# Kernel tuning notes

Hardware: AMD Instinct MI355X
Metric: run time of the kernel (lower is better)

Reference implementation:

```python
import jax, jax.numpy as jnp
import numpy as np

NUM_HEADS = 16


def setup_inputs() -> dict:
    key = jax.random.key(0)
    k1, k2, k3 = jax.random.split(key, 3)
    S, B, E = 2048, 4, 1024
    std = float(np.sqrt(2.0 / (E + E)))
    query = jax.random.normal(k1, (S, B, E), dtype=jnp.float32)
    in_proj_weight = jax.random.normal(k2, (3 * E, E), dtype=jnp.float32) * std
    in_proj_bias = jnp.zeros((3 * E,), dtype=jnp.float32)
    out_proj_weight = jax.random.normal(k3, (E, E), dtype=jnp.float32) * std
    out_proj_bias = jnp.zeros((E,), dtype=jnp.float32)
    return {
        "query": query,
        "in_proj_weight": in_proj_weight,
        "in_proj_bias": in_proj_bias,
        "out_proj_weight": out_proj_weight,
        "out_proj_bias": out_proj_bias,
    }


def reference(query, in_proj_weight, in_proj_bias, out_proj_weight, out_proj_bias):
    S, B, E = query.shape
    H = NUM_HEADS
    hd = E // H
    scale = hd ** -0.5
    # fused QKV projection: [S, B, 3E]
    lin = jnp.einsum("sbe,fe->sbf", query, in_proj_weight) + in_proj_bias
    # torch layout: view(S, B*H, 3, hd) -> interleaved [h, {q,k,v}, hd]
    lin = lin.reshape(S, B * H, 3, hd)
    q = lin[:, :, 0, :]  # [S, B*H, hd]
    k = lin[:, :, 1, :]
    v = lin[:, :, 2, :]
    # scores: [B*H, S_q, S_k]
    scores = jnp.einsum("sbd,tbd->bst", q, k) * scale
    attn = jax.nn.softmax(scores.astype(jnp.float32), axis=-1).astype(scores.dtype)
    # context: [S, B*H, hd] -> [S, B, E]
    ctx = jnp.einsum("bst,tbd->sbd", attn, v).reshape(S, B, E)
    out = jnp.einsum("sbe,fe->sbf", ctx, out_proj_weight) + out_proj_bias
    return out
```

## Files before the change

### kernel.cpp

```cpp
#include <hip/hip_runtime.h>
#include <hip/hip_bf16.h>

typedef __hip_bfloat16 bf16;
typedef __attribute__((ext_vector_type(8))) short short8;
typedef __attribute__((ext_vector_type(4))) float floatx4;

#define GLD_LDS(g, l) __builtin_amdgcn_global_load_lds( \
    (const __attribute__((address_space(1))) void*)(g), \
    (__attribute__((address_space(3))) void*)(l), 16, 0, 0)

#define CS 0.18033688f

__device__ __forceinline__ float fast_exp2(float x)
{
    const float fl = floorf(x);
    const float t  = x - fl;
    float p = 1.0f + t * (0.69583f + t * (0.22606f + t * 0.078024f));
    union { float f; int i; } u;
    u.f = p;
    u.i += ((int)fl) << 23;
    return u.f;
}

__global__ __launch_bounds__(256)
void cvt3_kernel(const float* __restrict__ q,  bf16* __restrict__ qo,
                 const float* __restrict__ w1, bf16* __restrict__ w1o,
                 const float* __restrict__ w2, bf16* __restrict__ w2o)
{
    const int i = blockIdx.x * 256 + threadIdx.x;
    const float* src; bf16* dst; long off;
    if (i < 1048576)       { src = q;  dst = qo;  off = (long)i * 8; }
    else if (i < 1441792)  { src = w1; dst = w1o; off = (long)(i - 1048576) * 8; }
    else                   { src = w2; dst = w2o; off = (long)(i - 1441792) * 8; }
    floatx4 a = *(const floatx4*)(src + off);
    floatx4 b = *(const floatx4*)(src + off + 4);
    short8 h;
    #pragma unroll
    for (int e = 0; e < 4; ++e) {
        union { bf16 v; short s; } u0, u1;
        u0.v = __float2bfloat16(a[e]); h[e]     = u0.s;
        u1.v = __float2bfloat16(b[e]); h[e + 4] = u1.s;
    }
    *(short8*)(dst + off) = h;
}

__device__ __forceinline__ void stage_f32(const float* __restrict__ src, int ld,
                                          bf16* lds, int t)
{
    const int sr = t >> 1;
    const int sc = (t & 1) * 16;
    const float* g = src + (long)sr * ld + sc;
    floatx4 f[4];
    #pragma unroll
    for (int i = 0; i < 4; ++i) f[i] = *(const floatx4*)(g + i * 4);
    short8 h[2];
    #pragma unroll
    for (int v = 0; v < 2; ++v)
        #pragma unroll
        for (int e = 0; e < 8; ++e) {
            union { bf16 b; short s; } u;
            u.b = __float2bfloat16(f[v * 2 + (e >> 2)][e & 3]);
            h[v][e] = u.s;
        }
    *(short8*)(lds + sr * 32 + sc)     = h[0];
    *(short8*)(lds + sr * 32 + sc + 8) = h[1];
}

template<int EPI, int AF32, int BF32>
__global__ __launch_bounds__(256, 2)
void gemm_bt(const void* __restrict__ Ap, const void* __restrict__ Bp,
             const float* __restrict__ bias,
             void* __restrict__ o0, bf16* __restrict__ o1, bf16* __restrict__ o2,
             int K, int N)
{
    __shared__ __align__(16) bf16 lA[2][128 * 32];
    __shared__ __align__(16) bf16 lB[2][128 * 32];

    const int t    = threadIdx.x;
    const int lane = t & 63;
    const int w    = t >> 6;

    const int nb   = N >> 7;
    const int lin  = blockIdx.y * nb + blockIdx.x;
    const int cpx  = (nb << 6) >> 3;
    const int swz  = (lin & 7) * cpx + (lin >> 3);
    const int mBase = (swz / nb) * 128;
    const int nBase = (swz % nb) * 128;

    const int wr = (w >> 1) * 64;
    const int wc = (w & 1) * 64;

    const int rowL = t >> 2;
    const int colL = (t & 3) * 8;
    const bf16* gA0 = (const bf16*)Ap + (long)(mBase + rowL) * K + colL;
    const bf16* gA1 = (const bf16*)Ap + (long)(mBase + rowL + 64) * K + colL;
    const bf16* gB0 = (const bf16*)Bp + (long)(nBase + rowL) * K + colL;
    const bf16* gB1 = (const bf16*)Bp + (long)(nBase + rowL + 64) * K + colL;
    const int ldst = w * 1024;

    floatx4 acc[4][4] = {};

    auto stage = [&](int buf, int k0) __attribute__((always_inline)) {
        if constexpr (AF32) {
            stage_f32((const float*)Ap + (long)mBase * K + k0, K, lA[buf], t);
        } else {
            GLD_LDS(gA0 + k0, (char*)lA[buf] + ldst);
            GLD_LDS(gA1 + k0, (char*)lA[buf] + ldst + 4096);
        }
        if constexpr (BF32) {
            stage_f32((const float*)Bp + (long)nBase * K + k0, K, lB[buf], t);
        } else {
            GLD_LDS(gB0 + k0, (char*)lB[buf] + ldst);
            GLD_LDS(gB1 + k0, (char*)lB[buf] + ldst + 4096);
        }
    };

    auto compute = [&](int buf) __attribute__((always_inline)) {
        short8 af[4], bfr[4];
        #pragma unroll
        for (int m = 0; m < 4; ++m)
            af[m] = *(const short8*)(lA[buf] + (wr + m * 16 + (lane & 15)) * 32 + (lane >> 4) * 8);
        #pragma unroll
        for (int n = 0; n < 4; ++n)
            bfr[n] = *(const short8*)(lB[buf] + (wc + n * 16 + (lane & 15)) * 32 + (lane >> 4) * 8);
        #pragma unroll
        for (int m = 0; m < 4; ++m)
            #pragma unroll
            for (int n = 0; n < 4; ++n)
                acc[m][n] = __builtin_amdgcn_mfma_f32_16x16x32_bf16(af[m], bfr[n], acc[m][n], 0, 0, 0);
    };

    stage(0, 0);
    asm volatile("s_waitcnt vmcnt(0)" ::: "memory");
    __syncthreads();

    for (int k0 = 0; k0 < K; k0 += 64) {
        if (k0 + 32 < K) stage(1, k0 + 32);
        compute(0);
        asm volatile("s_waitcnt vmcnt(0)" ::: "memory");
        __syncthreads();
        if (k0 + 32 < K) {
            if (k0 + 64 < K) stage(0, k0 + 64);
            compute(1);
            asm volatile("s_waitcnt vmcnt(0)" ::: "memory");
            __syncthreads();
        }
    }

    #pragma unroll
    for (int m = 0; m < 4; ++m) {
        #pragma unroll
        for (int n = 0; n < 4; ++n) {
            const int col = nBase + wc + n * 16 + (lane & 15);
            const int r0  = mBase + wr + m * 16 + ((lane >> 4) << 2);
            const float bv = bias[col];
            if constexpr (EPI == 0) {
                const int h   = col / 192;
                const int rem = col % 192;
                const int qkv = rem >> 6;
                const int d   = rem & 63;
                #pragma unroll
                for (int j = 0; j < 4; ++j) {
                    const int r = r0 + j;
                    const int s = r >> 2;
                    const int b = r & 3;
                    const float v = acc[m][n][j] + bv;
                    if (qkv == 0)
                        ((bf16*)o0)[(((((b << 4) + h) << 11) + s) << 6) + d] =
                            __float2bfloat16(v * CS);
                    else if (qkv == 1)
                        o1[(((((b << 4) + h) << 11) + s) << 6) + d] = __float2bfloat16(v);
                    else
                        o2[((((b << 4) + h) << 17)) + (d << 11) + s] = __float2bfloat16(v);
                }
            } else {
                #pragma unroll
                for (int j = 0; j < 4; ++j)
                    ((float*)o0)[(long)(r0 + j) * N + col] = acc[m][n][j] + bv;
            }
        }
    }
}

__global__ __launch_bounds__(256, 2)
void attn_kernel(const bf16* __restrict__ Q, const bf16* __restrict__ Kg,
                 const bf16* __restrict__ Vt, bf16* __restrict__ Ctx)
{
    __shared__ __align__(16) bf16 lK[2][64 * 64];
    __shared__ __align__(16) bf16 lV[2][64 * 64];

    const int t    = threadIdx.x;
    const int lane = t & 63;
    const int w    = t >> 6;
    const int f    = lane & 15;
    const int g    = lane >> 4;
    const int lin  = blockIdx.x;
    const int bh   = (lin & 7) | (((lin >> 8) & 7) << 3);
    const int q0   = ((lin >> 3) & 31) * 64 + w * 16;
    const long hb  = (long)bh * 2048 * 64;
    const bf16* Qh = Q  + hb;
    const bf16* Kh = Kg + hb;
    const bf16* Vh = Vt + hb;

    const bf16* kSrc[2]; const bf16* vSrc[2];
    #pragma unroll
    for (int i = 0; i < 2; ++i) {
        const int X = t * 16 + i * 4096;
        const int r = X >> 7;
        const int c = (X & 127) ^ ((r & 7) << 4);
        const int sr = (r & 3) | ((r & 16) >> 2) | ((r & 12) << 1) | (r & 32);
        kSrc[i] = Kh + sr * 64 + (c >> 1);
        vSrc[i] = Vh + r * 2048 + (c >> 1);
    }
    const int ldst = w * 1024;

    const int rb0 = (f * 128 + g * 16)      ^ ((f & 7) << 4);
    const int rb1 = (f * 128 + g * 16 + 64) ^ ((f & 7) << 4);

    short8 qf[2];
    #pragma unroll
    for (int kk = 0; kk < 2; ++kk)
        qf[kk] = *(const short8*)(Qh + (q0 + f) * 64 + kk * 32 + g * 8);

    short8 ones;
    #pragma unroll
    for (int e = 0; e < 8; ++e) ones[e] = (short)0x3F80;

    floatx4 o[4] = {};
    floatx4 dn = {};

    #pragma unroll
    for (int i = 0; i < 2; ++i) {
        GLD_LDS(kSrc[i], (char*)lK[0] + ldst + i * 4096);
        GLD_LDS(vSrc[i], (char*)lV[0] + ldst + i * 4096);
    }
    asm volatile("s_waitcnt vmcnt(0)" ::: "memory");
    __syncthreads();

    auto tile = [&](const bf16* curK, const bf16* curV,
                    bf16* nxtK, bf16* nxtV, int t0) __attribute__((always_inline)) {
        if (t0 + 64 < 2048) {
            const int ko = (t0 + 64) * 64;
            const int vo = t0 + 64;
            #pragma unroll
            for (int i = 0; i < 2; ++i) {
                GLD_LDS(kSrc[i] + ko, (char*)nxtK + ldst + i * 4096);
                GLD_LDS(vSrc[i] + vo, (char*)nxtV + ldst + i * 4096);
            }
        }

        short8 kf[4][2];
        #pragma unroll
        for (int n = 0; n < 4; ++n) {
            kf[n][0] = *(const short8*)((const char*)curK + rb0 + n * 2048);
            kf[n][1] = *(const short8*)((const char*)curK + rb1 + n * 2048);
        }

        floatx4 sa2[4] = {};
        __builtin_amdgcn_s_setprio(1);
        #pragma unroll
        for (int n = 0; n < 4; ++n)
            #pragma unroll
            for (int kk = 0; kk < 2; ++kk)
                sa2[n] = __builtin_amdgcn_mfma_f32_16x16x32_bf16(kf[n][kk], qf[kk], sa2[n], 0, 0, 0);
        __builtin_amdgcn_s_setprio(0);

        short8 vf[4][2];
        #pragma unroll
        for (int n2 = 0; n2 < 4; ++n2) {
            vf[n2][0] = *(const short8*)((const char*)curV + rb0 + n2 * 2048);
            vf[n2][1] = *(const short8*)((const char*)curV + rb1 + n2 * 2048);
        }

        short8 pf[2];
        #pragma unroll
        for (int kk = 0; kk < 2; ++kk) {
            union { int i4[4]; short8 s8; } u;
            #pragma unroll
            for (int v = 0; v < 4; ++v) {
                const int n = 2 * kk + (v >> 1);
                const int e = 2 * (v & 1);
                float2 pr;
                pr.x = fast_exp2(sa2[n][e]);
                pr.y = fast_exp2(sa2[n][e + 1]);
                __hip_bfloat162 pb = __float22bfloat162_rn(pr);
                u.i4[v] = *reinterpret_cast<int*>(&pb);
            }
            pf[kk] = u.s8;
        }

        __builtin_amdgcn_s_setprio(1);
        #pragma unroll
        for (int n2 = 0; n2 < 4; ++n2)
            #pragma unroll
            for (int kk = 0; kk < 2; ++kk)
                o[n2] = __builtin_amdgcn_mfma_f32_16x16x32_bf16(pf[kk], vf[n2][kk], o[n2], 0, 0, 0);
        #pragma unroll
        for (int kk = 0; kk < 2; ++kk)
            dn = __builtin_amdgcn_mfma_f32_16x16x32_bf16(pf[kk], ones, dn, 0, 0, 0);
        __builtin_amdgcn_s_setprio(0);

        __syncthreads();
    };

    for (int t0 = 0; t0 < 2048; t0 += 128) {
        tile(lK[0], lV[0], lK[1], lV[1], t0);
        tile(lK[1], lV[1], lK[0], lV[0], t0 + 64);
    }

    const int b = bh >> 4;
    const int h = bh & 15;
    float inv[4];
    #pragma unroll
    for (int j = 0; j < 4; ++j)
        inv[j] = 1.f / dn[j];
    #pragma unroll
    for (int n2 = 0; n2 < 4; ++n2) {
        const int dim = (h << 6) + n2 * 16 + f;
        #pragma unroll
        for (int j = 0; j < 4; ++j) {
            const int srw = q0 + (g << 2) + j;
            Ctx[(((srw << 2) + b) << 10) + dim] = __float2bfloat16(o[n2][j] * inv[j]);
        }
    }
}

extern "C" void kernel_launch(void* const* d_in, const int* in_sizes, int n_in,
                              void* d_out, int out_size, void* d_ws, size_t ws_size,
                              hipStream_t stream)
{
    const float* query = (const float*)d_in[0];
    const float* wIn   = (const float*)d_in[1];
    const float* bIn   = (const float*)d_in[2];
    const float* wOut  = (const float*)d_in[3];
    const float* bOut  = (const float*)d_in[4];

    const size_t HEADSZ = (size_t)64 * 2048 * 64;
    bf16* Qws = (bf16*)d_ws;
    bf16* Kws = Qws + HEADSZ;
    bf16* Vtw = Kws + HEADSZ;
    bf16* Ctx = Vtw + HEADSZ;
    bf16* qbf = Ctx;
    if (ws_size < 4 * HEADSZ * sizeof(bf16)) return;

    const size_t NEED_BIG = (4 * HEADSZ + 3145728 + 1048576) * sizeof(bf16);
    if (ws_size >= NEED_BIG) {
        bf16* wInBf  = Ctx + HEADSZ;
        bf16* wOutBf = wInBf + 3145728;
        cvt3_kernel<<<dim3(6144), 256, 0, stream>>>(query, qbf, wIn, wInBf, wOut, wOutBf);
        gemm_bt<0, 0, 0><<<dim3(24, 64), 256, 0, stream>>>(qbf, wInBf, bIn,
                                                           Qws, Kws, Vtw, 1024, 3072);
        attn_kernel<<<dim3(2048), 256, 0, stream>>>(Qws, Kws, Vtw, Ctx);
        gemm_bt<1, 0, 0><<<dim3(8, 64), 256, 0, stream>>>(Ctx, wOutBf, bOut,
                                                          d_out, nullptr, nullptr, 1024, 1024);
    } else {
        cvt3_kernel<<<dim3(4096), 256, 0, stream>>>(query, qbf, nullptr, nullptr, nullptr, nullptr);
        gemm_bt<0, 0, 1><<<dim3(24, 64), 256, 0, stream>>>(qbf, wIn, bIn,
                                                           Qws, Kws, Vtw, 1024, 3072);
        attn_kernel<<<dim3(2048), 256, 0, stream>>>(Qws, Kws, Vtw, Ctx);
        gemm_bt<1, 0, 1><<<dim3(8, 64), 256, 0, stream>>>(Ctx, wOut, bOut,
                                                          d_out, nullptr, nullptr, 1024, 1024);
    }
}
```

Baseline: 230.3 us.

## Triple-buffer K/V tiles in attention with partial vmcnt waits

The attention kernel moves from double-buffered to triple-buffered LDS for K and V tiles. It prefetches two tiles ahead and waits only on the older loads with s_waitcnt vmcnt(4) instead of draining all loads before each barrier. This hides more global-load latency behind the MFMA work. In exchange, LDS use grows from 32KB to 48KB per block, which could limit occupancy under the two-blocks-per-CU launch bound.

```diff
diff --git a/kernel.cpp b/kernel.cpp
--- a/kernel.cpp
+++ b/kernel.cpp
@@ -186,8 +186,8 @@
 void attn_kernel(const bf16* __restrict__ Q, const bf16* __restrict__ Kg,
                  const bf16* __restrict__ Vt, bf16* __restrict__ Ctx)
 {
-    __shared__ __align__(16) bf16 lK[2][64 * 64];
-    __shared__ __align__(16) bf16 lV[2][64 * 64];
+    __shared__ __align__(16) bf16 lK[3][64 * 64];
+    __shared__ __align__(16) bf16 lV[3][64 * 64];
 
     const int t    = threadIdx.x;
     const int lane = t & 63;
@@ -234,20 +234,29 @@
         GLD_LDS(kSrc[i], (char*)lK[0] + ldst + i * 4096);
         GLD_LDS(vSrc[i], (char*)lV[0] + ldst + i * 4096);
     }
-    asm volatile("s_waitcnt vmcnt(0)" ::: "memory");
-    __syncthreads();
-
-    auto tile = [&](const bf16* curK, const bf16* curV,
-                    bf16* nxtK, bf16* nxtV, int t0) __attribute__((always_inline)) {
-        if (t0 + 64 < 2048) {
-            const int ko = (t0 + 64) * 64;
-            const int vo = t0 + 64;
-            #pragma unroll
-            for (int i = 0; i < 2; ++i) {
-                GLD_LDS(kSrc[i] + ko, (char*)nxtK + ldst + i * 4096);
-                GLD_LDS(vSrc[i] + vo, (char*)nxtV + ldst + i * 4096);
+    #pragma unroll
+    for (int i = 0; i < 2; ++i) {
+        GLD_LDS(kSrc[i] + 64 * 64, (char*)lK[1] + ldst + i * 4096);
+        GLD_LDS(vSrc[i] + 64,      (char*)lV[1] + ldst + i * 4096);
+    }
+    asm volatile("s_waitcnt vmcnt(4)" ::: "memory");
+    __builtin_amdgcn_s_barrier();
+    __builtin_amdgcn_sched_barrier(0);
+
+    int cb = 0, sb = 2;
+    for (int i = 0; i < 32; ++i) {
+        if (i + 2 < 32) {
+            const int ko = (i + 2) * 64 * 64;
+            const int vo = (i + 2) * 64;
+            #pragma unroll
+            for (int ii = 0; ii < 2; ++ii) {
+                GLD_LDS(kSrc[ii] + ko, (char*)lK[sb] + ldst + ii * 4096);
+                GLD_LDS(vSrc[ii] + vo, (char*)lV[sb] + ldst + ii * 4096);
             }
         }
+
+        const bf16* curK = lK[cb];
+        const bf16* curV = lV[cb];
 
         short8 kf[4][2];
         #pragma unroll
@@ -300,12 +309,15 @@
             dn = __builtin_amdgcn_mfma_f32_16x16x32_bf16(pf[kk], ones, dn, 0, 0, 0);
         __builtin_amdgcn_s_setprio(0);
 
-        __syncthreads();
-    };
-
-    for (int t0 = 0; t0 < 2048; t0 += 128) {
-        tile(lK[0], lV[0], lK[1], lV[1], t0);
-        tile(lK[1], lV[1], lK[0], lV[0], t0 + 64);
+        if (i + 1 < 32) {
+            if (i + 2 < 32) asm volatile("s_waitcnt vmcnt(4)" ::: "memory");
+            else            asm volatile("s_waitcnt vmcnt(0)" ::: "memory");
+            __builtin_amdgcn_s_barrier();
+            __builtin_amdgcn_sched_barrier(0);
+        }
+
+        cb = (cb == 2) ? 0 : cb + 1;
+        sb = (sb == 2) ? 0 : sb + 1;
     }
 
     const int b = bh >> 4;
```

Measured after the change: 230.2 us. No clear change (-0.0%).
